# Optimization experiments

Measured on AMD Instinct MI355X. Metric: run time of the kernel, lower is better.

## Reference

```python
import jax, jax.numpy as jnp
import numpy as np
import math

D_MODEL = 1024
NUM_HEADS = 16
D_K = D_MODEL // NUM_HEADS
THETA = 10000.0
NEG_INF = 1.0e6  # module uses -1e6, not -inf


def _rope_tables(seq_len):
    pair_idx = jnp.arange(0, D_K, 2, dtype=jnp.float32)
    inv_freq = 1.0 / (THETA ** (pair_idx / D_K))
    pos = jnp.arange(seq_len, dtype=jnp.float32)
    angles = jnp.outer(pos, inv_freq)  # (S, D_K//2)
    return jnp.cos(angles), jnp.sin(angles)


def _apply_rope(x, cos, sin):
    # x: (B, H, S, D_K); cos/sin: (S, D_K//2)
    xe = x[..., 0::2]
    xo = x[..., 1::2]
    oe = xe * cos - xo * sin
    oo = xe * sin + xo * cos
    return jnp.stack([oe, oo], axis=-1).reshape(x.shape)


def setup_inputs() -> dict:
    key = jax.random.key(0)
    k0, k1, k2, k3, k4 = jax.random.split(key, 5)
    B, S = 2, 2048
    x = jax.random.normal(k0, (B, S, D_MODEL), dtype=jnp.float32)
    scale = 0.02
    wq = jax.random.normal(k1, (D_MODEL, D_MODEL), dtype=jnp.float32) * scale
    wk = jax.random.normal(k2, (D_MODEL, D_MODEL), dtype=jnp.float32) * scale
    wv = jax.random.normal(k3, (D_MODEL, D_MODEL), dtype=jnp.float32) * scale
    wo = jax.random.normal(k4, (D_MODEL, D_MODEL), dtype=jnp.float32) * scale
    return {"x": x, "wq": wq, "wk": wk, "wv": wv, "wo": wo}


def reference(x, wq, wk, wv, wo):
    B, S, _ = x.shape
    q = x @ wq.T
    k = x @ wk.T
    v = x @ wv.T
    # (B, S, H, d_k) -> (B, H, S, d_k)
    q = q.reshape(B, S, NUM_HEADS, D_K).transpose(0, 2, 1, 3)
    k = k.reshape(B, S, NUM_HEADS, D_K).transpose(0, 2, 1, 3)
    v = v.reshape(B, S, NUM_HEADS, D_K).transpose(0, 2, 1, 3)
    cos, sin = _rope_tables(S)
    q = _apply_rope(q, cos, sin)
    k = _apply_rope(k, cos, sin)
    scores = jnp.einsum("bhqd,bhkd->bhqk", q, k) / math.sqrt(D_K)
    causal = jnp.tril(jnp.ones((S, S), dtype=bool))
    scores = jnp.where(causal, scores, -NEG_INF)
    attn = jax.nn.softmax(scores, axis=-1)
    out = jnp.einsum("bhqk,bhkd->bhqd", attn, v)
    out = out.transpose(0, 2, 1, 3).reshape(B, S, D_MODEL)
    return out @ wo.T
```

## Files before the change

### kernel.cpp

```cpp
#include <hip/hip_runtime.h>

typedef __attribute__((ext_vector_type(8))) __bf16 bf16x8;
typedef __attribute__((ext_vector_type(8))) _Float16 f16x8;
typedef __attribute__((ext_vector_type(4))) float f32x4;
typedef __attribute__((ext_vector_type(8))) unsigned short u16x8;

#define MFMA_BF16(a, b, c) __builtin_amdgcn_mfma_f32_16x16x32_bf16((a), (b), (c), 0, 0, 0)
#define MFMA_F16(a, b, c)  __builtin_amdgcn_mfma_f32_16x16x32_f16((a), (b), (c), 0, 0, 0)
#define LOG2E 1.44269504088896340736f
#define QSCALE 0.18033688011112042f

__device__ __forceinline__ float b2f(unsigned short u) {
    union { unsigned int i; float f; } v; v.i = ((unsigned int)u) << 16; return v.f;
}
__device__ __forceinline__ unsigned short f2bf(float f) {
    union { float f; unsigned int i; } v; v.f = f;
    unsigned int u = v.i;
    return (unsigned short)((u + 0x7fffu + ((u >> 16) & 1u)) >> 16);
}

__device__ __forceinline__ void gl_lds16(const void* g, void* l) {
    __builtin_amdgcn_global_load_lds(
        (const __attribute__((address_space(1))) void*)g,
        (__attribute__((address_space(3))) void*)l,
        16, 0, 0);
}

__global__ __launch_bounds__(256) void cvt_all(const float* __restrict__ x,
                                               const float* __restrict__ wq,
                                               const float* __restrict__ wk,
                                               const float* __restrict__ wv,
                                               const float* __restrict__ wo,
                                               unsigned short* __restrict__ xb,
                                               unsigned short* __restrict__ wqb,
                                               unsigned short* __restrict__ wkb,
                                               unsigned short* __restrict__ wvb,
                                               unsigned short* __restrict__ wob) {
    int id = blockIdx.x * 256 + threadIdx.x;
    const float* src; unsigned short* dst; size_t off; float scl = 1.0f;
    if (id < 524288)      { src = x;  dst = xb;  off = (size_t)id * 8; }
    else if (id < 655360) { src = wq; dst = wqb; off = (size_t)(id - 524288) * 8; scl = QSCALE; }
    else if (id < 786432) { src = wk; dst = wkb; off = (size_t)(id - 655360) * 8; }
    else if (id < 917504) { src = wv; dst = wvb; off = (size_t)(id - 786432) * 8; }
    else                  { src = wo; dst = wob; off = (size_t)(id - 917504) * 8; }
    float4 a = *(const float4*)(src + off);
    float4 b = *(const float4*)(src + off + 4);
    u16x8 o;
    o[0] = f2bf(a.x * scl); o[1] = f2bf(a.y * scl); o[2] = f2bf(a.z * scl); o[3] = f2bf(a.w * scl);
    o[4] = f2bf(b.x * scl); o[5] = f2bf(b.y * scl); o[6] = f2bf(b.z * scl); o[7] = f2bf(b.w * scl);
    *(u16x8*)(dst + off) = o;
}

template <int MODE>
__device__ __forceinline__ void gemm128_bt(const unsigned short* __restrict__ A,
                                           const unsigned short* __restrict__ B,
                                           void* __restrict__ Cv,
                                           int m0, int n0, int ldc,
                                           unsigned short* As, unsigned short* Bs) {
    const int tid = threadIdx.x;
    const int w = tid >> 6, lane = tid & 63;
    const int quad = lane >> 4, l15 = lane & 15;
    const int wm = w & 1, wn = w >> 1;

    f32x4 acc[4][4];
#pragma unroll
    for (int mt = 0; mt < 4; ++mt)
#pragma unroll
        for (int nt = 0; nt < 4; ++nt) acc[mt][nt] = f32x4{0.f, 0.f, 0.f, 0.f};

    for (int k0 = 0; k0 < 1024; k0 += 32) {
        __syncthreads();
#pragma unroll
        for (int i = 0; i < 2; ++i) {
            int L = (w * 2 + i) * 64 + lane;
            int r = L >> 2;
            int c = (L & 3) ^ ((r >> 1) & 3);
            gl_lds16(A + (size_t)(m0 + r) * 1024 + k0 + c * 8, As + L * 8);
            gl_lds16(B + (size_t)(n0 + r) * 1024 + k0 + c * 8, Bs + L * 8);
        }
        __syncthreads();

        bf16x8 af[4], bfr[4];
#pragma unroll
        for (int mt = 0; mt < 4; ++mt) {
            int row = wm * 64 + mt * 16 + l15;
            af[mt] = *(const bf16x8*)(As + row * 32 + (quad ^ ((row >> 1) & 3)) * 8);
        }
#pragma unroll
        for (int nt = 0; nt < 4; ++nt) {
            int row = wn * 64 + nt * 16 + l15;
            bfr[nt] = *(const bf16x8*)(Bs + row * 32 + (quad ^ ((row >> 1) & 3)) * 8);
        }
#pragma unroll
        for (int mt = 0; mt < 4; ++mt)
#pragma unroll
            for (int nt = 0; nt < 4; ++nt)
                acc[mt][nt] = MFMA_BF16(af[mt], bfr[nt], acc[mt][nt]);
    }

    float invf[4], sgn = 0.f;
    if constexpr (MODE == 3) {
        sgn = (l15 & 1) ? 1.0f : -1.0f;
#pragma unroll
        for (int nt = 0; nt < 4; ++nt)
            invf[nt] = exp2f(-0.41524101186092029f * (float)((nt * 16 + l15) >> 1));
    }

#pragma unroll
    for (int mt = 0; mt < 4; ++mt) {
        int grow = m0 + wm * 64 + mt * 16 + quad * 4;
#pragma unroll
        for (int nt = 0; nt < 4; ++nt) {
            int gcol = n0 + wn * 64 + nt * 16 + l15;
#pragma unroll
            for (int r = 0; r < 4; ++r) {
                float val = acc[mt][nt][r];
                size_t idx = (size_t)(grow + r) * ldc + gcol;
                if constexpr (MODE == 0) {
                    ((unsigned short*)Cv)[idx] = f2bf(val);
                } else if constexpr (MODE == 1) {
                    ((float*)Cv)[idx] = val;
                } else if constexpr (MODE == 2) {
                    _Float16 hv = (_Float16)val;
                    ((unsigned short*)Cv)[idx] = __builtin_bit_cast(unsigned short, hv);
                } else {
                    float p = __shfl_xor(val, 1);
                    float pos = (float)((grow + r) & 2047);
                    float ang = pos * invf[nt];
                    float out = val * __cosf(ang) + sgn * p * __sinf(ang);
                    ((unsigned short*)Cv)[idx] = f2bf(out);
                }
            }
        }
    }
}

__global__ __launch_bounds__(256) void gemm_qkv(const unsigned short* __restrict__ X,
                                                const unsigned short* __restrict__ Wq,
                                                const unsigned short* __restrict__ Wk,
                                                const unsigned short* __restrict__ Wv,
                                                unsigned short* __restrict__ Qo,
                                                unsigned short* __restrict__ Ko,
                                                unsigned short* __restrict__ Vt) {
    __shared__ unsigned short As[128 * 32];
    __shared__ unsigned short Bs[128 * 32];
    int y = blockIdx.y;
    if (y < 16) {
        int sel = y >> 3;
        int m0 = blockIdx.x * 128;
        int n0 = (y & 7) * 128;
        const unsigned short* B = sel ? Wk : Wq;
        unsigned short* C = sel ? Ko : Qo;
        gemm128_bt<3>(X, B, C, m0, n0, 1024, As, Bs);
    } else {
        int m0 = (y & 7) * 128;
        int n0 = blockIdx.x * 128;
        gemm128_bt<2>(Wv, X, Vt, m0, n0, 4096, As, Bs);
    }
}

__global__ __launch_bounds__(256) void gemm_out(const unsigned short* __restrict__ A,
                                                const unsigned short* __restrict__ Wo,
                                                float* __restrict__ C) {
    __shared__ unsigned short As[128 * 32];
    __shared__ unsigned short Bs[128 * 32];
    gemm128_bt<1>(A, Wo, C, blockIdx.x * 128, blockIdx.y * 128, 1024, As, Bs);
}

#define FBODY(KB, MASKED)                                                               \
    {                                                                                   \
        const int kb_ = (KB);                                                           \
        f32x4 sc[4];                                                                    \
        _Pragma("unroll")                                                               \
        for (int nt = 0; nt < 4; ++nt) {                                                \
            int row = nt * 16 + l15;                                                    \
            int cof = (quad ^ (row & 7)) * 8;                                           \
            bf16x8 kf0 = *(const bf16x8*)(Ks + row * 64 + cof);                         \
            bf16x8 kf1 = *(const bf16x8*)(Ks + row * 64 + (cof ^ 32));                  \
            f32x4 z = f32x4{0.f, 0.f, 0.f, 0.f};                                        \
            sc[nt] = MFMA_BF16(qf0, kf0, z);                                            \
            sc[nt] = MFMA_BF16(qf1, kf1, sc[nt]);                                       \
        }                                                                               \
        unsigned short* Pw = Ps[w];                                                     \
        _Pragma("unroll")                                                               \
        for (int nt = 0; nt < 4; ++nt) {                                                \
            float e[4];                                                                 \
            _Pragma("unroll")                                                           \
            for (int r = 0; r < 4; ++r) {                                               \
                float ev = exp2f(sc[nt][r]);                                            \
                if (MASKED) {                                                           \
                    int kpos = kb_ * 64 + nt * 16 + l15;                                \
                    int qpos = qpos0 + quad * 4 + r;                                    \
                    ev = (kpos > qpos) ? 0.f : ev;                                      \
                }                                                                       \
                e[r] = ev;                                                              \
            }                                                                           \
            unsigned pk01 = __builtin_bit_cast(unsigned,                                \
                                __builtin_amdgcn_cvt_pkrtz(e[0], e[1]));                \
            unsigned pk23 = __builtin_bit_cast(unsigned,                                \
                                __builtin_amdgcn_cvt_pkrtz(e[2], e[3]));                \
            int col = nt * 16 + l15;                                                    \
            Pw[(quad * 4 + 0) * 72 + col] = (unsigned short)pk01;                       \
            Pw[(quad * 4 + 1) * 72 + col] = (unsigned short)(pk01 >> 16);               \
            Pw[(quad * 4 + 2) * 72 + col] = (unsigned short)pk23;                       \
            Pw[(quad * 4 + 3) * 72 + col] = (unsigned short)(pk23 >> 16);               \
        }                                                                               \
        __asm__ volatile("s_waitcnt lgkmcnt(0)" ::: "memory");                          \
        f16x8 pf0 = *(const f16x8*)(Pw + l15 * 72 + quad * 8);                          \
        f16x8 pf1 = *(const f16x8*)(Pw + l15 * 72 + 32 + quad * 8);                     \
        lacc = MFMA_F16(pf0, ones, lacc);                                               \
        lacc = MFMA_F16(pf1, ones, lacc);                                               \
        _Pragma("unroll")                                                               \
        for (int nt = 0; nt < 4; ++nt) {                                                \
            int row = nt * 16 + l15;                                                    \
            int cof = (quad ^ (row & 7)) * 8;                                           \
            f16x8 vf0 = *(const f16x8*)(Vs + row * 64 + cof);                           \
            f16x8 vf1 = *(const f16x8*)(Vs + row * 64 + (cof ^ 32));                    \
            accO[nt] = MFMA_F16(pf0, vf0, accO[nt]);                                    \
            accO[nt] = MFMA_F16(pf1, vf1, accO[nt]);                                    \
        }                                                                               \
    }

__global__ __launch_bounds__(256) void flash_attn(const unsigned short* __restrict__ Q,
                                                  const unsigned short* __restrict__ Kb,
                                                  const unsigned short* __restrict__ Vt,
                                                  unsigned short* __restrict__ O) {
    int id = blockIdx.x;
    int xcd = id & 7;
    int sl = id >> 3;
    int rr = sl >> 5;
    int j  = sl & 31;
    int qt;
    if (rr == 0)      qt = j;
    else if (rr == 1) qt = 31 - j;
    else if (rr == 2) qt = (j + 16) & 31;
    else              qt = 31 - ((j + 16) & 31);
    int bh = xcd + 8 * rr;
    int b = bh >> 4, h = bh & 15;
    int tid = threadIdx.x, w = tid >> 6, lane = tid & 63;
    int quad = lane >> 4, l15 = lane & 15;
    int qrow0 = b * 2048 + qt * 64 + w * 16;
    int qpos0 = qt * 64 + w * 16;

    __shared__ unsigned short Ks[64 * 64];
    __shared__ unsigned short Vs[64 * 64];
    __shared__ unsigned short Ps[4][16 * 72];

    bf16x8 qf0, qf1;
    {
        const unsigned short* qp = Q + (size_t)(qrow0 + l15) * 1024 + h * 64 + quad * 8;
        qf0 = *(const bf16x8*)qp;
        qf1 = *(const bf16x8*)(qp + 32);
    }
    f16x8 ones;
#pragma unroll
    for (int jj = 0; jj < 8; ++jj) ones[jj] = (_Float16)1.0f;

    int L0 = w * 128 + lane;
    int L1 = L0 + 64;
    int r0 = L0 >> 3, c0s = (L0 & 7) ^ (r0 & 7);
    int r1 = L1 >> 3, c1s = (L1 & 7) ^ (r1 & 7);
    const unsigned short* Kg0 = Kb + (size_t)(b * 2048 + r0) * 1024 + h * 64 + c0s * 8;
    const unsigned short* Kg1 = Kb + (size_t)(b * 2048 + r1) * 1024 + h * 64 + c1s * 8;
    const unsigned short* Vg0 = Vt + (size_t)(h * 64 + r0) * 4096 + b * 2048 + c0s * 8;
    const unsigned short* Vg1 = Vt + (size_t)(h * 64 + r1) * 4096 + b * 2048 + c1s * 8;

    f32x4 accO[4];
#pragma unroll
    for (int nt = 0; nt < 4; ++nt) accO[nt] = f32x4{0.f, 0.f, 0.f, 0.f};
    f32x4 lacc = f32x4{0.f, 0.f, 0.f, 0.f};

    for (int kb = 0; kb <= qt; ++kb) {
        __syncthreads();
        {
            size_t ko = (size_t)kb * 64 * 1024;
            size_t vo = (size_t)kb * 64;
            gl_lds16(Kg0 + ko, Ks + L0 * 8);
            gl_lds16(Kg1 + ko, Ks + L1 * 8);
            gl_lds16(Vg0 + vo, Vs + L0 * 8);
            gl_lds16(Vg1 + vo, Vs + L1 * 8);
        }
        __syncthreads();
        if (kb < qt) {
            FBODY(kb, 0)
        } else {
            FBODY(kb, 1)
        }
    }

    float inv[4];
#pragma unroll
    for (int r = 0; r < 4; ++r) inv[r] = 1.0f / lacc[r];
#pragma unroll
    for (int nt = 0; nt < 4; ++nt)
#pragma unroll
        for (int r = 0; r < 4; ++r)
            O[(size_t)(qrow0 + quad * 4 + r) * 1024 + h * 64 + nt * 16 + l15] =
                f2bf(accO[nt][r] * inv[r]);
}

extern "C" void kernel_launch(void* const* d_in, const int* in_sizes, int n_in,
                              void* d_out, int out_size, void* d_ws, size_t ws_size,
                              hipStream_t stream) {
    (void)in_sizes; (void)n_in; (void)out_size; (void)ws_size;
    const float* x  = (const float*)d_in[0];
    const float* wq = (const float*)d_in[1];
    const float* wk = (const float*)d_in[2];
    const float* wv = (const float*)d_in[3];
    const float* wo = (const float*)d_in[4];
    float* out = (float*)d_out;

    const size_t T = (size_t)4096 * 1024;
    const size_t W = (size_t)1024 * 1024;
    unsigned short* Q   = (unsigned short*)d_ws;
    unsigned short* K   = Q + T;
    unsigned short* Vt  = K + T;
    unsigned short* xb  = Vt + T;
    unsigned short* AO  = xb;
    unsigned short* wqb = xb + T;
    unsigned short* wkb = wqb + W;
    unsigned short* wvb = wkb + W;
    unsigned short* wob = wvb + W;

    cvt_all  <<<dim3(4096),   256, 0, stream>>>(x, wq, wk, wv, wo, xb, wqb, wkb, wvb, wob);
    gemm_qkv <<<dim3(32, 24), 256, 0, stream>>>(xb, wqb, wkb, wvb, Q, K, Vt);
    flash_attn<<<dim3(1024),  256, 0, stream>>>(Q, K, Vt, AO);
    gemm_out <<<dim3(32, 8),  256, 0, stream>>>(AO, wob, out);
}
```

Before: 183.7 us.

## Restructure flash attention: 128-row Q tiles, double-buffered KV, register-resident P

Each wave now handles 32 query rows instead of 16, so every K/V fragment loaded from LDS feeds two MFMAs. Scores are computed transposed (K as the A operand), which puts the probabilities into the register layout the PV MFMA needs and removes the LDS round trip for P. K/V tiles are double-buffered, with the next tile's global-to-LDS load issued before the current tile's compute, so one barrier per iteration replaces two. Each of the 256 blocks processes a balanced pair of causal Q tiles (j and 15-j). The cost is higher register pressure and fewer blocks, which may reduce occupancy and latency hiding.

```diff
diff --git a/kernel.cpp b/kernel.cpp
--- a/kernel.cpp
+++ b/kernel.cpp
@@ -2,8 +2,10 @@
 
 typedef __attribute__((ext_vector_type(8))) __bf16 bf16x8;
 typedef __attribute__((ext_vector_type(8))) _Float16 f16x8;
+typedef __attribute__((ext_vector_type(4))) _Float16 f16x4;
 typedef __attribute__((ext_vector_type(4))) float f32x4;
 typedef __attribute__((ext_vector_type(8))) unsigned short u16x8;
+typedef __attribute__((ext_vector_type(4))) unsigned int u32x4;
 
 #define MFMA_BF16(a, b, c) __builtin_amdgcn_mfma_f32_16x16x32_bf16((a), (b), (c), 0, 0, 0)
 #define MFMA_F16(a, b, c)  __builtin_amdgcn_mfma_f32_16x16x32_f16((a), (b), (c), 0, 0, 0)
@@ -167,57 +169,69 @@
     gemm128_bt<1>(A, Wo, C, blockIdx.x * 128, blockIdx.y * 128, 1024, As, Bs);
 }
 
-#define FBODY(KB, MASKED)                                                               \
+#define FBODY(MASKED)                                                                   \
     {                                                                                   \
-        const int kb_ = (KB);                                                           \
-        f32x4 sc[4];                                                                    \
+        bf16x8 kf[4][2];                                                                \
         _Pragma("unroll")                                                               \
         for (int nt = 0; nt < 4; ++nt) {                                                \
             int row = nt * 16 + l15;                                                    \
-            int cof = (quad ^ (row & 7)) * 8;                                           \
-            bf16x8 kf0 = *(const bf16x8*)(Ks + row * 64 + cof);                         \
-            bf16x8 kf1 = *(const bf16x8*)(Ks + row * 64 + (cof ^ 32));                  \
-            f32x4 z = f32x4{0.f, 0.f, 0.f, 0.f};                                        \
-            sc[nt] = MFMA_BF16(qf0, kf0, z);                                            \
-            sc[nt] = MFMA_BF16(qf1, kf1, sc[nt]);                                       \
+            const char* kp = (const char*)Ksb + row * 128;                              \
+            int swk = row & 7;                                                          \
+            kf[nt][0] = *(const bf16x8*)(kp + ((quad ^ swk) << 4));                     \
+            kf[nt][1] = *(const bf16x8*)(kp + (((quad ^ 4) ^ swk) << 4));               \
         }                                                                               \
-        unsigned short* Pw = Ps[w];                                                     \
+        f16x8 pf[2][2];                                                                 \
+        _Pragma("unroll")                                                               \
+        for (int mt = 0; mt < 2; ++mt) {                                                \
+            f32x4 sc[4];                                                                \
+            _Pragma("unroll")                                                           \
+            for (int nt = 0; nt < 4; ++nt) {                                            \
+                f32x4 z = f32x4{0.f, 0.f, 0.f, 0.f};                                    \
+                z = MFMA_BF16(kf[nt][0], qf[mt][0], z);                                 \
+                sc[nt] = MFMA_BF16(kf[nt][1], qf[mt][1], z);                            \
+            }                                                                           \
+            int qpos = qposw + mt * 16 + l15;                                           \
+            unsigned pk[8];                                                             \
+            _Pragma("unroll")                                                           \
+            for (int nt = 0; nt < 4; ++nt) {                                            \
+                float e[4];                                                             \
+                _Pragma("unroll")                                                       \
+                for (int r = 0; r < 4; ++r) {                                           \
+                    float ev = exp2f(sc[nt][r]);                                        \
+                    if (MASKED) {                                                       \
+                        int kpos = kb * 64 + nt * 16 + quad * 4 + r;                    \
+                        ev = (kpos > qpos) ? 0.f : ev;                                  \
+                    }                                                                   \
+                    e[r] = ev;                                                          \
+                }                                                                       \
+                pk[nt * 2 + 0] = __builtin_bit_cast(unsigned,                           \
+                                     __builtin_amdgcn_cvt_pkrtz(e[0], e[1]));           \
+                pk[nt * 2 + 1] = __builtin_bit_cast(unsigned,                           \
+                                     __builtin_amdgcn_cvt_pkrtz(e[2], e[3]));           \
+            }                                                                           \
+            u32x4 pw0 = u32x4{pk[0], pk[1], pk[2], pk[3]};                              \
+            u32x4 pw1 = u32x4{pk[4], pk[5], pk[6], pk[7]};                              \
+            pf[mt][0] = __builtin_bit_cast(f16x8, pw0);                                 \
+            pf[mt][1] = __builtin_bit_cast(f16x8, pw1);                                 \
+            lacc[mt] = MFMA_F16(pf[mt][0], ones, lacc[mt]);                             \
+            lacc[mt] = MFMA_F16(pf[mt][1], ones, lacc[mt]);                             \
+        }                                                                               \
         _Pragma("unroll")                                                               \
         for (int nt = 0; nt < 4; ++nt) {                                                \
-            float e[4];                                                                 \
-            _Pragma("unroll")                                                           \
-            for (int r = 0; r < 4; ++r) {                                               \
-                float ev = exp2f(sc[nt][r]);                                            \
-                if (MASKED) {                                                           \
-                    int kpos = kb_ * 64 + nt * 16 + l15;                                \
-                    int qpos = qpos0 + quad * 4 + r;                                    \
-                    ev = (kpos > qpos) ? 0.f : ev;                                      \
-                }                                                                       \
-                e[r] = ev;                                                              \
-            }                                                                           \
-            unsigned pk01 = __builtin_bit_cast(unsigned,                                \
-                                __builtin_amdgcn_cvt_pkrtz(e[0], e[1]));                \
-            unsigned pk23 = __builtin_bit_cast(unsigned,                                \
-                                __builtin_amdgcn_cvt_pkrtz(e[2], e[3]));                \
-            int col = nt * 16 + l15;                                                    \
-            Pw[(quad * 4 + 0) * 72 + col] = (unsigned short)pk01;                       \
-            Pw[(quad * 4 + 1) * 72 + col] = (unsigned short)(pk01 >> 16);               \
-            Pw[(quad * 4 + 2) * 72 + col] = (unsigned short)pk23;                       \
-            Pw[(quad * 4 + 3) * 72 + col] = (unsigned short)(pk23 >> 16);               \
-        }                                                                               \
-        __asm__ volatile("s_waitcnt lgkmcnt(0)" ::: "memory");                          \
-        f16x8 pf0 = *(const f16x8*)(Pw + l15 * 72 + quad * 8);                          \
-        f16x8 pf1 = *(const f16x8*)(Pw + l15 * 72 + 32 + quad * 8);                     \
-        lacc = MFMA_F16(pf0, ones, lacc);                                               \
-        lacc = MFMA_F16(pf1, ones, lacc);                                               \
-        _Pragma("unroll")                                                               \
-        for (int nt = 0; nt < 4; ++nt) {                                                \
-            int row = nt * 16 + l15;                                                    \
-            int cof = (quad ^ (row & 7)) * 8;                                           \
-            f16x8 vf0 = *(const f16x8*)(Vs + row * 64 + cof);                           \
-            f16x8 vf1 = *(const f16x8*)(Vs + row * 64 + (cof ^ 32));                    \
-            accO[nt] = MFMA_F16(pf0, vf0, accO[nt]);                                    \
-            accO[nt] = MFMA_F16(pf1, vf1, accO[nt]);                                    \
+            int rowd = nt * 16 + l15;                                                   \
+            const char* vp = (const char*)Vsb + rowd * 128;                             \
+            int swv = rowd & 7;                                                         \
+            int qh = quad >> 1, sub = (quad & 1) * 8;                                   \
+            f16x4 a0 = *(const f16x4*)(vp + (((qh + 0) ^ swv) << 4) + sub);             \
+            f16x4 a1 = *(const f16x4*)(vp + (((qh + 2) ^ swv) << 4) + sub);             \
+            f16x8 v0 = __builtin_shufflevector(a0, a1, 0, 1, 2, 3, 4, 5, 6, 7);         \
+            accO[0][nt] = MFMA_F16(pf[0][0], v0, accO[0][nt]);                          \
+            accO[1][nt] = MFMA_F16(pf[1][0], v0, accO[1][nt]);                          \
+            f16x4 b0 = *(const f16x4*)(vp + (((qh + 4) ^ swv) << 4) + sub);             \
+            f16x4 b1 = *(const f16x4*)(vp + (((qh + 6) ^ swv) << 4) + sub);             \
+            f16x8 v1 = __builtin_shufflevector(b0, b1, 0, 1, 2, 3, 4, 5, 6, 7);         \
+            accO[0][nt] = MFMA_F16(pf[0][1], v1, accO[0][nt]);                          \
+            accO[1][nt] = MFMA_F16(pf[1][1], v1, accO[1][nt]);                          \
         }                                                                               \
     }
 
@@ -228,75 +242,101 @@
     int id = blockIdx.x;
     int xcd = id & 7;
     int sl = id >> 3;
-    int rr = sl >> 5;
-    int j  = sl & 31;
-    int qt;
-    if (rr == 0)      qt = j;
-    else if (rr == 1) qt = 31 - j;
-    else if (rr == 2) qt = (j + 16) & 31;
-    else              qt = 31 - ((j + 16) & 31);
+    int rr = sl >> 3;
+    int j  = sl & 7;
     int bh = xcd + 8 * rr;
     int b = bh >> 4, h = bh & 15;
     int tid = threadIdx.x, w = tid >> 6, lane = tid & 63;
     int quad = lane >> 4, l15 = lane & 15;
-    int qrow0 = b * 2048 + qt * 64 + w * 16;
-    int qpos0 = qt * 64 + w * 16;
-
-    __shared__ unsigned short Ks[64 * 64];
-    __shared__ unsigned short Vs[64 * 64];
-    __shared__ unsigned short Ps[4][16 * 72];
-
-    bf16x8 qf0, qf1;
-    {
-        const unsigned short* qp = Q + (size_t)(qrow0 + l15) * 1024 + h * 64 + quad * 8;
-        qf0 = *(const bf16x8*)qp;
-        qf1 = *(const bf16x8*)(qp + 32);
-    }
-    f16x8 ones;
-#pragma unroll
-    for (int jj = 0; jj < 8; ++jj) ones[jj] = (_Float16)1.0f;
+
+    __shared__ unsigned short Ks[2 * 4096];
+    __shared__ unsigned short Vs[2 * 4096];
 
     int L0 = w * 128 + lane;
     int L1 = L0 + 64;
-    int r0 = L0 >> 3, c0s = (L0 & 7) ^ (r0 & 7);
-    int r1 = L1 >> 3, c1s = (L1 & 7) ^ (r1 & 7);
-    const unsigned short* Kg0 = Kb + (size_t)(b * 2048 + r0) * 1024 + h * 64 + c0s * 8;
-    const unsigned short* Kg1 = Kb + (size_t)(b * 2048 + r1) * 1024 + h * 64 + c1s * 8;
-    const unsigned short* Vg0 = Vt + (size_t)(h * 64 + r0) * 4096 + b * 2048 + c0s * 8;
-    const unsigned short* Vg1 = Vt + (size_t)(h * 64 + r1) * 4096 + b * 2048 + c1s * 8;
-
-    f32x4 accO[4];
-#pragma unroll
-    for (int nt = 0; nt < 4; ++nt) accO[nt] = f32x4{0.f, 0.f, 0.f, 0.f};
-    f32x4 lacc = f32x4{0.f, 0.f, 0.f, 0.f};
-
-    for (int kb = 0; kb <= qt; ++kb) {
-        __syncthreads();
-        {
-            size_t ko = (size_t)kb * 64 * 1024;
-            size_t vo = (size_t)kb * 64;
-            gl_lds16(Kg0 + ko, Ks + L0 * 8);
-            gl_lds16(Kg1 + ko, Ks + L1 * 8);
-            gl_lds16(Vg0 + vo, Vs + L0 * 8);
-            gl_lds16(Vg1 + vo, Vs + L1 * 8);
-        }
-        __syncthreads();
-        if (kb < qt) {
-            FBODY(kb, 0)
-        } else {
-            FBODY(kb, 1)
-        }
-    }
-
-    float inv[4];
-#pragma unroll
-    for (int r = 0; r < 4; ++r) inv[r] = 1.0f / lacc[r];
-#pragma unroll
-    for (int nt = 0; nt < 4; ++nt)
-#pragma unroll
-        for (int r = 0; r < 4; ++r)
-            O[(size_t)(qrow0 + quad * 4 + r) * 1024 + h * 64 + nt * 16 + l15] =
-                f2bf(accO[nt][r] * inv[r]);
+    int r0 = L0 >> 3, c0 = (L0 & 7) ^ (r0 & 7);
+    int r1 = L1 >> 3, c1 = (L1 & 7) ^ (r1 & 7);
+    const unsigned short* Kg0 = Kb + (size_t)(b * 2048 + r0) * 1024 + h * 64 + c0 * 8;
+    const unsigned short* Kg1 = Kb + (size_t)(b * 2048 + r1) * 1024 + h * 64 + c1 * 8;
+    const unsigned short* Vg0 = Vt + (size_t)(h * 64 + r0) * 4096 + b * 2048 + c0 * 8;
+    const unsigned short* Vg1 = Vt + (size_t)(h * 64 + r1) * 4096 + b * 2048 + c1 * 8;
+
+    f16x8 ones;
+#pragma unroll
+    for (int t = 0; t < 8; ++t) ones[t] = (_Float16)1.0f;
+
+#define STAGE(kb_, buf_)                                                    \
+    {                                                                       \
+        size_t ko = (size_t)(kb_) * 64 * 1024;                              \
+        size_t vo = (size_t)(kb_) * 64;                                     \
+        unsigned short* kd = Ks + (buf_) * 4096;                            \
+        unsigned short* vd = Vs + (buf_) * 4096;                            \
+        gl_lds16(Kg0 + ko, kd + L0 * 8);                                    \
+        gl_lds16(Kg1 + ko, kd + L1 * 8);                                    \
+        gl_lds16(Vg0 + vo, vd + L0 * 8);                                    \
+        gl_lds16(Vg1 + vo, vd + L1 * 8);                                    \
+    }
+
+    for (int tp = 0; tp < 2; ++tp) {
+        int qt = tp ? (15 - j) : j;
+        int qrow0 = b * 2048 + qt * 128 + w * 32;
+        int qposw = qt * 128 + w * 32;
+        int nkb = 2 * qt + 2;
+
+        STAGE(0, 0)
+
+        bf16x8 qf[2][2];
+#pragma unroll
+        for (int mt = 0; mt < 2; ++mt) {
+            const unsigned short* qp =
+                Q + (size_t)(qrow0 + mt * 16 + l15) * 1024 + h * 64 + quad * 8;
+            qf[mt][0] = *(const bf16x8*)qp;
+            qf[mt][1] = *(const bf16x8*)(qp + 32);
+        }
+
+        f32x4 accO[2][4];
+        f32x4 lacc[2];
+#pragma unroll
+        for (int mt = 0; mt < 2; ++mt) {
+            lacc[mt] = f32x4{0.f, 0.f, 0.f, 0.f};
+#pragma unroll
+            for (int nt = 0; nt < 4; ++nt) accO[mt][nt] = f32x4{0.f, 0.f, 0.f, 0.f};
+        }
+
+        __asm__ volatile("s_waitcnt vmcnt(0)" ::: "memory");
+        __builtin_amdgcn_s_barrier();
+        __builtin_amdgcn_sched_barrier(0);
+
+        int cur = 0;
+        for (int kb = 0; kb < nkb; ++kb) {
+            if (kb + 1 < nkb) STAGE(kb + 1, cur ^ 1)
+            const unsigned short* Ksb = Ks + cur * 4096;
+            const unsigned short* Vsb = Vs + cur * 4096;
+            if (kb < nkb - 2) {
+                FBODY(0)
+            } else {
+                FBODY(1)
+            }
+            __asm__ volatile("s_waitcnt vmcnt(0)" ::: "memory");
+            __builtin_amdgcn_s_barrier();
+            __builtin_amdgcn_sched_barrier(0);
+            cur ^= 1;
+        }
+
+#pragma unroll
+        for (int mt = 0; mt < 2; ++mt) {
+            float inv[4];
+#pragma unroll
+            for (int r = 0; r < 4; ++r) inv[r] = 1.0f / lacc[mt][r];
+#pragma unroll
+            for (int nt = 0; nt < 4; ++nt)
+#pragma unroll
+                for (int r = 0; r < 4; ++r)
+                    O[(size_t)(qrow0 + mt * 16 + quad * 4 + r) * 1024 +
+                      h * 64 + nt * 16 + l15] = f2bf(accO[mt][nt][r] * inv[r]);
+        }
+    }
+#undef STAGE
 }
 
 extern "C" void kernel_launch(void* const* d_in, const int* in_sizes, int n_in,
@@ -324,6 +364,6 @@
 
     cvt_all  <<<dim3(4096),   256, 0, stream>>>(x, wq, wk, wv, wo, xb, wqb, wkb, wvb, wob);
     gemm_qkv <<<dim3(32, 24), 256, 0, stream>>>(xb, wqb, wkb, wvb, Q, K, Vt);
-    flash_attn<<<dim3(1024),  256, 0, stream>>>(Q, K, Vt, AO);
+    flash_attn<<<dim3(256),   256, 0, stream>>>(Q, K, Vt, AO);
     gemm_out <<<dim3(32, 8),  256, 0, stream>>>(AO, wob, out);
 }
```

Result: no change. 187.4 us (+2.0%).
